# Optimization experiments

Hardware: AMD Instinct MI355X
Metric: run time of the kernel (lower is better)

## Reference

```python
import jax, jax.numpy as jnp
import numpy as np

N_NODES = 50000
N_EDGES = 800000
D = 128  # d_feat == hidden_channels


def setup_inputs() -> dict:
    key = jax.random.key(0)
    ks = jax.random.split(key, 7)
    s = 1.0 / np.sqrt(D)
    return {
        "x": jax.random.normal(ks[0], (N_NODES, D), dtype=jnp.float32),
        "edge_index": jax.random.randint(ks[1], (2, N_EDGES), 0, N_NODES, dtype=jnp.int64),
        "W1_l": jax.random.normal(ks[2], (D, D), dtype=jnp.float32) * s,
        "b1": jnp.zeros((D,), dtype=jnp.float32),
        "W1_r": jax.random.normal(ks[3], (D, D), dtype=jnp.float32) * s,
        "W2_l": jax.random.normal(ks[4], (D, D), dtype=jnp.float32) * s,
        "b2": jnp.zeros((D,), dtype=jnp.float32),
        "W2_r": jax.random.normal(ks[5], (D, D), dtype=jnp.float32) * s,
    }


def reference(x, edge_index, W1_l, b1, W1_r, W2_l, b2, W2_r):
    src = edge_index[0]
    dst = edge_index[1]
    n = x.shape[0]
    # in-degree for mean aggregation (zero-degree nodes get 0 aggregate)
    deg = jax.ops.segment_sum(jnp.ones_like(src, dtype=x.dtype), dst, num_segments=n)
    inv_deg = (1.0 / jnp.maximum(deg, 1.0))[:, None]  # [N,1]

    def sage_conv(h, Wl, b, Wr):
        # mean over incoming neighbor messages, then lin_l(agg) + lin_r(h)
        agg = jax.ops.segment_sum(h[src], dst, num_segments=n) * inv_deg  # [N,D]
        return agg @ Wl + b + h @ Wr

    h = jax.nn.relu(sage_conv(x, W1_l, b1, W1_r))
    return sage_conv(h, W2_l, b2, W2_r)
```

## Files before the change

kernel.cpp:

```cpp
#include <hip/hip_runtime.h>
#include <hip/hip_bf16.h>

typedef __attribute__((ext_vector_type(8))) short bf16x8;
typedef __attribute__((ext_vector_type(4))) float f32x4;
typedef __attribute__((ext_vector_type(2))) float f32x2;

#define CAP 64
#define SH  8

static __device__ inline unsigned short f2b(float f) {
    unsigned u = __float_as_uint(f);
    unsigned r = (u + 0x7FFFu + ((u >> 16) & 1u)) >> 16;
    return (unsigned short)r;
}
static __device__ inline float blo(unsigned u) { return __uint_as_float(u << 16); }
static __device__ inline float bhi(unsigned u) { return __uint_as_float(u & 0xFFFF0000u); }

__global__ void zero_kernel(int* __restrict__ p, int n) {
    int i = blockIdx.x * blockDim.x + threadIdx.x;
    if (i < n) p[i] = 0;
}

__global__ __launch_bounds__(256) void fill_shard_kernel(
        const int* __restrict__ ei, int* __restrict__ cursor,
        unsigned short* __restrict__ edge16, int E, int N, int G, int npg) {
    int s = blockIdx.x & (SH - 1);
    int i = blockIdx.x >> 3;
    int d_lo = s * npg;
    int d_hi = d_lo + npg; if (d_hi > N) d_hi = N;
    int C = (E + G - 1) / G;
    int e0 = i * C;
    int e1 = e0 + C; if (e1 > E) e1 = E;
    for (int e = e0 + threadIdx.x; e < e1; e += 256) {
        int d = ei[E + e];
        if (d < d_lo || d >= d_hi) continue;
        int src = ei[e];
        if ((unsigned)src >= (unsigned)N) src = 0;
        int pos = atomicAdd(&cursor[d], 1);
        if (pos < CAP) edge16[(size_t)d * CAP + pos] = (unsigned short)src;
    }
}

__global__ __launch_bounds__(256) void x2b_kernel(const float* __restrict__ x,
                                                  unsigned short* __restrict__ xb,
                                                  int n4) {
    int i = blockIdx.x * blockDim.x + threadIdx.x;
    if (i >= n4) return;
    float4 v = ((const float4*)x)[i];
    ushort4 b;
    b.x = f2b(v.x); b.y = f2b(v.y); b.z = f2b(v.z); b.w = f2b(v.w);
    ((ushort4*)xb)[i] = b;
}

__global__ __launch_bounds__(256) void aggregate_kernel(
        const unsigned short* __restrict__ in, const int* __restrict__ cursor,
        const unsigned short* __restrict__ edge16, const int* __restrict__ ei,
        unsigned short* __restrict__ agg, int E, int N) {
    int tid  = threadIdx.x;
    int wave = tid >> 6;
    int lane = tid & 63;
    int g    = lane >> 4;
    int fl   = lane & 15;
    int node = blockIdx.x * 16 + wave * 4 + g;
    if (node >= N) return;
    int deg = cursor[node];

    f32x2 a01 = {0.f, 0.f}, a23 = {0.f, 0.f}, a45 = {0.f, 0.f}, a67 = {0.f, 0.f};

    if (deg <= CAP) {
        const unsigned short* base = edge16 + (size_t)node * CAP;
        int idx[4];
        #pragma unroll
        for (int c = 0; c < 4; ++c) idx[c] = (int)base[c * 16 + fl];
        #pragma unroll
        for (int c = 0; c < 4; ++c) {
            int j0 = c * 16;
            if (deg <= j0) break;
            int jend = deg < j0 + 16 ? deg : j0 + 16;
            for (int j = j0; j < jend; ++j) {
                int s = __shfl(idx[c], (g << 4) | (j - j0));
                const uint4 v = *(const uint4*)(in + (size_t)s * 128 + fl * 8);
                a01 += (f32x2){blo(v.x), bhi(v.x)};
                a23 += (f32x2){blo(v.y), bhi(v.y)};
                a45 += (f32x2){blo(v.z), bhi(v.z)};
                a67 += (f32x2){blo(v.w), bhi(v.w)};
            }
        }
    } else {
        for (int j = 0; j < E; ++j) {
            if (ei[E + j] == node) {
                int s = ei[j];
                if ((unsigned)s >= (unsigned)N) s = 0;
                const uint4 v = *(const uint4*)(in + (size_t)s * 128 + fl * 8);
                a01 += (f32x2){blo(v.x), bhi(v.x)};
                a23 += (f32x2){blo(v.y), bhi(v.y)};
                a45 += (f32x2){blo(v.z), bhi(v.z)};
                a67 += (f32x2){blo(v.w), bhi(v.w)};
            }
        }
    }

    float inv = 1.0f / (float)(deg > 1 ? deg : 1);
    uint4 o;
    o.x = (unsigned)f2b(a01.x * inv) | ((unsigned)f2b(a01.y * inv) << 16);
    o.y = (unsigned)f2b(a23.x * inv) | ((unsigned)f2b(a23.y * inv) << 16);
    o.z = (unsigned)f2b(a45.x * inv) | ((unsigned)f2b(a45.y * inv) << 16);
    o.w = (unsigned)f2b(a67.x * inv) | ((unsigned)f2b(a67.y * inv) << 16);
    *(uint4*)(agg + (size_t)node * 128 + fl * 8) = o;
}

__global__ void prep_w_kernel(const float* __restrict__ W1l, const float* __restrict__ W1r,
                              const float* __restrict__ W2l, const float* __restrict__ W2r,
                              unsigned short* __restrict__ wt) {
    int n = blockIdx.x & 127;
    int layer = blockIdx.x >> 7;
    int k = threadIdx.x;
    const float* Wlp = layer ? W2l : W1l;
    const float* Wrp = layer ? W2r : W1r;
    unsigned short* dst = wt + (size_t)layer * 128 * 256 + (size_t)n * 256;
    dst[k]       = f2b(Wlp[(size_t)k * 128 + n]);
    dst[k + 128] = f2b(Wrp[(size_t)k * 128 + n]);
}

template<int RELU, int OUT_BF16>
__global__ __launch_bounds__(256) void gemm_mfma_kernel(
        const unsigned short* __restrict__ Arow, const unsigned short* __restrict__ Xrow,
        const unsigned short* __restrict__ Wt, const float* __restrict__ bias,
        void* __restrict__ outp, int n) {
    constexpr int LDK = 264;
    __shared__ unsigned short sA[64 * LDK];
    int tid = threadIdx.x;
    int row0 = blockIdx.x * 64;

    #pragma unroll
    for (int it = 0; it < 8; ++it) {
        int c = tid + it * 256;
        int r = c >> 5;
        int q = c & 31;
        int row = row0 + r; if (row >= n) row = n - 1;
        uint4 v = (q < 16) ? ((const uint4*)(Arow + (size_t)row * 128))[q]
                           : ((const uint4*)(Xrow + (size_t)row * 128))[q - 16];
        *(uint4*)&sA[r * LDK + q * 8] = v;
    }
    __syncthreads();

    int lane = tid & 63;
    int wave = tid >> 6;
    int quad = lane >> 4;
    int tm   = lane & 15;

    f32x4 acc[4][2];
    #pragma unroll
    for (int m = 0; m < 4; ++m)
        #pragma unroll
        for (int j = 0; j < 2; ++j)
            acc[m][j] = (f32x4){0.f, 0.f, 0.f, 0.f};

    const unsigned short* wb0 = Wt + (size_t)(wave * 32 + tm) * 256;

    #pragma unroll
    for (int ks = 0; ks < 8; ++ks) {
        int k0 = ks * 32 + quad * 8;
        bf16x8 a[4], b[2];
        #pragma unroll
        for (int m = 0; m < 4; ++m)
            a[m] = *(const bf16x8*)&sA[(m * 16 + tm) * LDK + k0];
        #pragma unroll
        for (int j = 0; j < 2; ++j)
            b[j] = *(const bf16x8*)(wb0 + (size_t)j * 16 * 256 + k0);
        #pragma unroll
        for (int m = 0; m < 4; ++m)
            #pragma unroll
            for (int j = 0; j < 2; ++j)
                acc[m][j] = __builtin_amdgcn_mfma_f32_16x16x32_bf16(a[m], b[j], acc[m][j], 0, 0, 0);
    }

    #pragma unroll
    for (int j = 0; j < 2; ++j) {
        int ncol = wave * 32 + j * 16 + tm;
        float bb = bias[ncol];
        #pragma unroll
        for (int m = 0; m < 4; ++m) {
            #pragma unroll
            for (int reg = 0; reg < 4; ++reg) {
                int row = row0 + m * 16 + quad * 4 + reg;
                if (row >= n) continue;
                float v = acc[m][j][reg] + bb;
                if (RELU) v = v > 0.f ? v : 0.f;
                if (OUT_BF16)
                    ((unsigned short*)outp)[(size_t)row * 128 + ncol] = f2b(v);
                else
                    ((float*)outp)[(size_t)row * 128 + ncol] = v;
            }
        }
    }
}

extern "C" void kernel_launch(void* const* d_in, const int* in_sizes, int n_in,
                              void* d_out, int out_size, void* d_ws, size_t ws_size,
                              hipStream_t stream) {
    const float* x   = (const float*)d_in[0];
    const int*   ei  = (const int*)d_in[1];
    const float* W1l = (const float*)d_in[2];
    const float* b1  = (const float*)d_in[3];
    const float* W1r = (const float*)d_in[4];
    const float* W2l = (const float*)d_in[5];
    const float* b2  = (const float*)d_in[6];
    const float* W2r = (const float*)d_in[7];
    float* out = (float*)d_out;

    const int D = 128;
    const int N = in_sizes[0] / D;
    const int E = in_sizes[1] / 2;

    char* ws = (char*)d_ws;
    size_t off = 0;
    auto alloc = [&](size_t bytes) {
        size_t o = off;
        off = (off + bytes + 511) & ~(size_t)511;
        return (void*)(ws + o);
    };
    int*            cursor  = (int*)           alloc((size_t)N * 4);
    unsigned short* edge16  = (unsigned short*)alloc((size_t)N * CAP * 2);
    unsigned short* agg_bf  = (unsigned short*)alloc((size_t)N * D * 2);
    unsigned short* xb      = (unsigned short*)alloc((size_t)N * D * 2);
    unsigned short* wt      = (unsigned short*)alloc((size_t)2 * 128 * 256 * 2);
    unsigned short* h_bf = xb;
    (void)ws_size; (void)n_in; (void)out_size;

    zero_kernel<<<(N + 255) / 256, 256, 0, stream>>>(cursor, N);
    {
        int G = 256;
        int npg = (N + SH - 1) / SH;
        fill_shard_kernel<<<SH * G, 256, 0, stream>>>(ei, cursor, edge16, E, N, G, npg);
    }

    int n4 = N * D / 4;
    x2b_kernel<<<(n4 + 255) / 256, 256, 0, stream>>>(x, xb, n4);
    prep_w_kernel<<<256, 128, 0, stream>>>(W1l, W1r, W2l, W2r, wt);
    const unsigned short* wt1 = wt;
    const unsigned short* wt2 = wt + (size_t)128 * 256;

    int agg_grid  = (N + 15) / 16;
    int gemm_grid = (N + 63) / 64;

    aggregate_kernel<<<agg_grid, 256, 0, stream>>>(xb, cursor, edge16, ei, agg_bf, E, N);
    gemm_mfma_kernel<1, 1><<<gemm_grid, 256, 0, stream>>>(agg_bf, xb, wt1, b1, (void*)h_bf, N);

    aggregate_kernel<<<agg_grid, 256, 0, stream>>>(h_bf, cursor, edge16, ei, agg_bf, E, N);
    gemm_mfma_kernel<0, 0><<<gemm_grid, 256, 0, stream>>>(agg_bf, h_bf, wt2, b2, (void*)out, N);
}
```

Before: 229.5 us.

## Fuse neighbor aggregation into MFMA GEMM kernel and merge prep kernels

Each layer now builds the mean-aggregated neighbor rows directly into shared memory inside the GEMM block, alongside the self rows. This removes the bf16 agg buffer round-trip through global memory and two launches per layer. The zero, x-to-bf16 and weight-transpose kernels are merged into one launch. The cost is that the gather-heavy aggregation now shares a block with the MFMA phase, which changes occupancy. Each block covers 64 nodes in 4 serial batches, so there is less gather parallelism per block. A separate h buffer is now allocated because the input can no longer be overwritten in place.

```diff
diff --git a/kernel.cpp b/kernel.cpp
--- a/kernel.cpp
+++ b/kernel.cpp
@@ -16,9 +16,34 @@
 static __device__ inline float blo(unsigned u) { return __uint_as_float(u << 16); }
 static __device__ inline float bhi(unsigned u) { return __uint_as_float(u & 0xFFFF0000u); }
 
-__global__ void zero_kernel(int* __restrict__ p, int n) {
-    int i = blockIdx.x * blockDim.x + threadIdx.x;
-    if (i < n) p[i] = 0;
+__global__ __launch_bounds__(256) void prep_kernel(
+        const float* __restrict__ x, unsigned short* __restrict__ xb, int n4,
+        int* __restrict__ cursor, int N,
+        const float* __restrict__ W1l, const float* __restrict__ W1r,
+        const float* __restrict__ W2l, const float* __restrict__ W2r,
+        unsigned short* __restrict__ wt, int nbx, int nbz) {
+    int b = blockIdx.x, tid = threadIdx.x;
+    if (b < nbx) {
+        int i = b * 256 + tid;
+        if (i < n4) {
+            float4 v = ((const float4*)x)[i];
+            ushort4 o;
+            o.x = f2b(v.x); o.y = f2b(v.y); o.z = f2b(v.z); o.w = f2b(v.w);
+            ((ushort4*)xb)[i] = o;
+        }
+    } else if (b < nbx + nbz) {
+        int i = (b - nbx) * 256 + tid;
+        if (i < N) cursor[i] = 0;
+    } else {
+        int bb = b - nbx - nbz;
+        int layer = bb >> 7, n = bb & 127;
+        int k = tid & 127;
+        const float* Wlp = layer ? W2l : W1l;
+        const float* Wrp = layer ? W2r : W1r;
+        unsigned short* dst = wt + (size_t)layer * 32768 + (size_t)n * 256;
+        if (tid < 128) dst[k]       = f2b(Wlp[(size_t)k * 128 + n]);
+        else           dst[k + 128] = f2b(Wrp[(size_t)k * 128 + n]);
+    }
 }
 
 __global__ __launch_bounds__(256) void fill_shard_kernel(
@@ -41,111 +66,80 @@
     }
 }
 
-__global__ __launch_bounds__(256) void x2b_kernel(const float* __restrict__ x,
-                                                  unsigned short* __restrict__ xb,
-                                                  int n4) {
-    int i = blockIdx.x * blockDim.x + threadIdx.x;
-    if (i >= n4) return;
-    float4 v = ((const float4*)x)[i];
-    ushort4 b;
-    b.x = f2b(v.x); b.y = f2b(v.y); b.z = f2b(v.z); b.w = f2b(v.w);
-    ((ushort4*)xb)[i] = b;
-}
-
-__global__ __launch_bounds__(256) void aggregate_kernel(
+template<int RELU, int OUT_BF16>
+__global__ __launch_bounds__(256) void layer_kernel(
         const unsigned short* __restrict__ in, const int* __restrict__ cursor,
         const unsigned short* __restrict__ edge16, const int* __restrict__ ei,
-        unsigned short* __restrict__ agg, int E, int N) {
+        const unsigned short* __restrict__ Wt, const float* __restrict__ bias,
+        void* __restrict__ outp, int n, int E) {
+    constexpr int LDK = 264;
+    __shared__ unsigned short sA[64 * LDK];
     int tid  = threadIdx.x;
     int wave = tid >> 6;
     int lane = tid & 63;
-    int g    = lane >> 4;
-    int fl   = lane & 15;
-    int node = blockIdx.x * 16 + wave * 4 + g;
-    if (node >= N) return;
-    int deg = cursor[node];
-
-    f32x2 a01 = {0.f, 0.f}, a23 = {0.f, 0.f}, a45 = {0.f, 0.f}, a67 = {0.f, 0.f};
-
-    if (deg <= CAP) {
-        const unsigned short* base = edge16 + (size_t)node * CAP;
-        int idx[4];
-        #pragma unroll
-        for (int c = 0; c < 4; ++c) idx[c] = (int)base[c * 16 + fl];
-        #pragma unroll
-        for (int c = 0; c < 4; ++c) {
-            int j0 = c * 16;
-            if (deg <= j0) break;
-            int jend = deg < j0 + 16 ? deg : j0 + 16;
-            for (int j = j0; j < jend; ++j) {
-                int s = __shfl(idx[c], (g << 4) | (j - j0));
-                const uint4 v = *(const uint4*)(in + (size_t)s * 128 + fl * 8);
-                a01 += (f32x2){blo(v.x), bhi(v.x)};
-                a23 += (f32x2){blo(v.y), bhi(v.y)};
-                a45 += (f32x2){blo(v.z), bhi(v.z)};
-                a67 += (f32x2){blo(v.w), bhi(v.w)};
+    int row0 = blockIdx.x * 64;
+
+    #pragma unroll
+    for (int it = 0; it < 4; ++it) {
+        int c = tid + it * 256;
+        int r = c >> 4;
+        int q = c & 15;
+        int row = row0 + r; if (row >= n) row = n - 1;
+        uint4 v = ((const uint4*)(in + (size_t)row * 128))[q];
+        *(uint4*)&sA[r * LDK + 128 + q * 8] = v;
+    }
+
+    int g  = lane >> 4;
+    int fl = lane & 15;
+    for (int batch = 0; batch < 4; ++batch) {
+        int r = batch * 16 + wave * 4 + g;
+        int node = row0 + r;
+        if (node < n) {
+            int deg = cursor[node];
+            f32x2 a01 = {0.f,0.f}, a23 = {0.f,0.f}, a45 = {0.f,0.f}, a67 = {0.f,0.f};
+            if (deg <= CAP) {
+                const unsigned short* base = edge16 + (size_t)node * CAP;
+                int idx[4];
+                #pragma unroll
+                for (int c = 0; c < 4; ++c) idx[c] = (int)base[c * 16 + fl];
+                #pragma unroll
+                for (int c = 0; c < 4; ++c) {
+                    int j0 = c * 16;
+                    if (deg <= j0) break;
+                    int jend = deg < j0 + 16 ? deg : j0 + 16;
+                    for (int j = j0; j < jend; ++j) {
+                        int s = __shfl(idx[c], (g << 4) | (j - j0));
+                        const uint4 v = *(const uint4*)(in + (size_t)s * 128 + fl * 8);
+                        a01 += (f32x2){blo(v.x), bhi(v.x)};
+                        a23 += (f32x2){blo(v.y), bhi(v.y)};
+                        a45 += (f32x2){blo(v.z), bhi(v.z)};
+                        a67 += (f32x2){blo(v.w), bhi(v.w)};
+                    }
+                }
+            } else {
+                for (int j = 0; j < E; ++j) {
+                    if (ei[E + j] == node) {
+                        int s = ei[j];
+                        if ((unsigned)s >= (unsigned)n) s = 0;
+                        const uint4 v = *(const uint4*)(in + (size_t)s * 128 + fl * 8);
+                        a01 += (f32x2){blo(v.x), bhi(v.x)};
+                        a23 += (f32x2){blo(v.y), bhi(v.y)};
+                        a45 += (f32x2){blo(v.z), bhi(v.z)};
+                        a67 += (f32x2){blo(v.w), bhi(v.w)};
+                    }
+                }
             }
+            float inv = 1.0f / (float)(deg > 1 ? deg : 1);
+            uint4 o;
+            o.x = (unsigned)f2b(a01.x * inv) | ((unsigned)f2b(a01.y * inv) << 16);
+            o.y = (unsigned)f2b(a23.x * inv) | ((unsigned)f2b(a23.y * inv) << 16);
+            o.z = (unsigned)f2b(a45.x * inv) | ((unsigned)f2b(a45.y * inv) << 16);
+            o.w = (unsigned)f2b(a67.x * inv) | ((unsigned)f2b(a67.y * inv) << 16);
+            *(uint4*)&sA[r * LDK + fl * 8] = o;
         }
-    } else {
-        for (int j = 0; j < E; ++j) {
-            if (ei[E + j] == node) {
-                int s = ei[j];
-                if ((unsigned)s >= (unsigned)N) s = 0;
-                const uint4 v = *(const uint4*)(in + (size_t)s * 128 + fl * 8);
-                a01 += (f32x2){blo(v.x), bhi(v.x)};
-                a23 += (f32x2){blo(v.y), bhi(v.y)};
-                a45 += (f32x2){blo(v.z), bhi(v.z)};
-                a67 += (f32x2){blo(v.w), bhi(v.w)};
-            }
-        }
-    }
-
-    float inv = 1.0f / (float)(deg > 1 ? deg : 1);
-    uint4 o;
-    o.x = (unsigned)f2b(a01.x * inv) | ((unsigned)f2b(a01.y * inv) << 16);
-    o.y = (unsigned)f2b(a23.x * inv) | ((unsigned)f2b(a23.y * inv) << 16);
-    o.z = (unsigned)f2b(a45.x * inv) | ((unsigned)f2b(a45.y * inv) << 16);
-    o.w = (unsigned)f2b(a67.x * inv) | ((unsigned)f2b(a67.y * inv) << 16);
-    *(uint4*)(agg + (size_t)node * 128 + fl * 8) = o;
-}
-
-__global__ void prep_w_kernel(const float* __restrict__ W1l, const float* __restrict__ W1r,
-                              const float* __restrict__ W2l, const float* __restrict__ W2r,
-                              unsigned short* __restrict__ wt) {
-    int n = blockIdx.x & 127;
-    int layer = blockIdx.x >> 7;
-    int k = threadIdx.x;
-    const float* Wlp = layer ? W2l : W1l;
-    const float* Wrp = layer ? W2r : W1r;
-    unsigned short* dst = wt + (size_t)layer * 128 * 256 + (size_t)n * 256;
-    dst[k]       = f2b(Wlp[(size_t)k * 128 + n]);
-    dst[k + 128] = f2b(Wrp[(size_t)k * 128 + n]);
-}
-
-template<int RELU, int OUT_BF16>
-__global__ __launch_bounds__(256) void gemm_mfma_kernel(
-        const unsigned short* __restrict__ Arow, const unsigned short* __restrict__ Xrow,
-        const unsigned short* __restrict__ Wt, const float* __restrict__ bias,
-        void* __restrict__ outp, int n) {
-    constexpr int LDK = 264;
-    __shared__ unsigned short sA[64 * LDK];
-    int tid = threadIdx.x;
-    int row0 = blockIdx.x * 64;
-
-    #pragma unroll
-    for (int it = 0; it < 8; ++it) {
-        int c = tid + it * 256;
-        int r = c >> 5;
-        int q = c & 31;
-        int row = row0 + r; if (row >= n) row = n - 1;
-        uint4 v = (q < 16) ? ((const uint4*)(Arow + (size_t)row * 128))[q]
-                           : ((const uint4*)(Xrow + (size_t)row * 128))[q - 16];
-        *(uint4*)&sA[r * LDK + q * 8] = v;
     }
     __syncthreads();
 
-    int lane = tid & 63;
-    int wave = tid >> 6;
     int quad = lane >> 4;
     int tm   = lane & 15;
 
@@ -222,31 +216,28 @@
     };
     int*            cursor  = (int*)           alloc((size_t)N * 4);
     unsigned short* edge16  = (unsigned short*)alloc((size_t)N * CAP * 2);
-    unsigned short* agg_bf  = (unsigned short*)alloc((size_t)N * D * 2);
     unsigned short* xb      = (unsigned short*)alloc((size_t)N * D * 2);
+    unsigned short* h_bf    = (unsigned short*)alloc((size_t)N * D * 2);
     unsigned short* wt      = (unsigned short*)alloc((size_t)2 * 128 * 256 * 2);
-    unsigned short* h_bf = xb;
     (void)ws_size; (void)n_in; (void)out_size;
 
-    zero_kernel<<<(N + 255) / 256, 256, 0, stream>>>(cursor, N);
+    const unsigned short* wt1 = wt;
+    const unsigned short* wt2 = wt + (size_t)128 * 256;
+
+    int n4  = N * D / 4;
+    int nbx = (n4 + 255) / 256;
+    int nbz = (N + 255) / 256;
+    prep_kernel<<<nbx + nbz + 256, 256, 0, stream>>>(
+        x, xb, n4, cursor, N, W1l, W1r, W2l, W2r, wt, nbx, nbz);
+
     {
         int G = 256;
         int npg = (N + SH - 1) / SH;
         fill_shard_kernel<<<SH * G, 256, 0, stream>>>(ei, cursor, edge16, E, N, G, npg);
     }
 
-    int n4 = N * D / 4;
-    x2b_kernel<<<(n4 + 255) / 256, 256, 0, stream>>>(x, xb, n4);
-    prep_w_kernel<<<256, 128, 0, stream>>>(W1l, W1r, W2l, W2r, wt);
-    const unsigned short* wt1 = wt;
-    const unsigned short* wt2 = wt + (size_t)128 * 256;
-
-    int agg_grid  = (N + 15) / 16;
-    int gemm_grid = (N + 63) / 64;
-
-    aggregate_kernel<<<agg_grid, 256, 0, stream>>>(xb, cursor, edge16, ei, agg_bf, E, N);
-    gemm_mfma_kernel<1, 1><<<gemm_grid, 256, 0, stream>>>(agg_bf, xb, wt1, b1, (void*)h_bf, N);
-
-    aggregate_kernel<<<agg_grid, 256, 0, stream>>>(h_bf, cursor, edge16, ei, agg_bf, E, N);
-    gemm_mfma_kernel<0, 0><<<gemm_grid, 256, 0, stream>>>(agg_bf, h_bf, wt2, b2, (void*)out, N);
-}
+    int grid = (N + 63) / 64;
+
+    layer_kernel<1, 1><<<grid, 256, 0, stream>>>(xb,   cursor, edge16, ei, wt1, b1, (void*)h_bf, N, E);
+    layer_kernel<0, 0><<<grid, 256, 0, stream>>>(h_bf, cursor, edge16, ei, wt2, b2, (void*)out,  N, E);
+}
```

Result: slower. 241.3 us (+5.1%).
